# Optimization experiments

Measured on AMD Instinct MI355X. Metric: run time of the kernel, lower is better.

## Reference

```python
import jax, jax.numpy as jnp
import numpy as np

IN, HID, BATCH = 1024, 1024, 4096


def _linear_params(key, out_dim, in_dim):
    # torch.nn.Linear default init: U(-1/sqrt(in), 1/sqrt(in))
    k1, k2 = jax.random.split(key)
    bound = 1.0 / np.sqrt(in_dim)
    w = jax.random.uniform(k1, (out_dim, in_dim), jnp.float32, -bound, bound)
    b = jax.random.uniform(k2, (out_dim,), jnp.float32, -bound, bound)
    return w, b


def setup_inputs() -> dict:
    key = jax.random.key(0)
    keys = jax.random.split(key, 11)
    inp = {
        'input': jax.random.normal(keys[0], (BATCH, IN), jnp.float32),
        'h': jax.random.normal(keys[1], (BATCH, HID), jnp.float32),
        'c': jax.random.normal(keys[2], (BATCH, HID), jnp.float32),
    }
    names = ['i_i', 'i_h', 'f_i', 'f_h', 'g_i', 'g_h', 'o_i', 'o_h']
    for n, k in zip(names, keys[3:]):
        in_dim = IN if n.endswith('_i') else HID
        w, b = _linear_params(k, HID, in_dim)
        inp['w_' + n] = w
        inp['b_' + n] = b
    return inp


def reference(input, h, c,
              w_i_i, b_i_i, w_i_h, b_i_h,
              w_f_i, b_f_i, w_f_h, b_f_h,
              w_g_i, b_g_i, w_g_h, b_g_h,
              w_o_i, b_o_i, w_o_h, b_o_h):
    def lin(x, w, b):
        return x @ w.T + b

    i = jax.nn.sigmoid(lin(input, w_i_i, b_i_i) + lin(h, w_i_h, b_i_h))
    f = jax.nn.sigmoid(lin(input, w_f_i, b_f_i) + lin(h, w_f_h, b_f_h))
    g = jnp.tanh(lin(input, w_g_i, b_g_i) + lin(h, w_g_h, b_g_h))
    o = jax.nn.sigmoid(lin(input, w_o_i, b_o_i) + lin(h, w_o_h, b_o_h))
    c_prime = f * c + i * g
    h_prime = o * jnp.tanh(c_prime)
    return (h_prime, c_prime)
```

## Files before the change

### kernel.cpp

```cpp
#include <hip/hip_runtime.h>
#include <stdint.h>

#define BATCH 4096
#define IN_DIM 1024
#define HID 1024
#define KDIM 2048
#define NGATE 4096

typedef __attribute__((ext_vector_type(4))) float floatx4;
typedef __attribute__((ext_vector_type(8))) __bf16 bf16x8;

__device__ __forceinline__ unsigned short f2bf(float f) {
    union { float f; unsigned int u; } v; v.f = f;
    unsigned int u = v.u;
    u += 0x7fffu + ((u >> 16) & 1u);
    return (unsigned short)(u >> 16);
}
__device__ __forceinline__ float bf2f(unsigned short s) {
    union { unsigned int u; float f; } v; v.u = ((unsigned int)s) << 16;
    return v.f;
}

__global__ void prep_kernel(
    const float* __restrict__ x,  const float* __restrict__ h,
    const float* __restrict__ wii, const float* __restrict__ wih,
    const float* __restrict__ wfi, const float* __restrict__ wfh,
    const float* __restrict__ wgi, const float* __restrict__ wgh,
    const float* __restrict__ woi, const float* __restrict__ woh,
    const float* __restrict__ bii, const float* __restrict__ bih,
    const float* __restrict__ bfi, const float* __restrict__ bfh,
    const float* __restrict__ bgi, const float* __restrict__ bgh,
    const float* __restrict__ boi, const float* __restrict__ boh,
    unsigned short* __restrict__ Xb,
    unsigned short* __restrict__ Wb,
    float* __restrict__ bias)
{
    const int t = blockIdx.x * blockDim.x + threadIdx.x;
    const int XV = BATCH * KDIM / 4;
    if (t < XV) {
        const int e = t * 4;
        const int b = e >> 11, k = e & 2047;
        const float* src = (k < IN_DIM) ? (x + (size_t)b * IN_DIM + k)
                                        : (h + (size_t)b * HID + (k - IN_DIM));
        float4 v = *(const float4*)src;
        ushort4 o = { f2bf(v.x), f2bf(v.y), f2bf(v.z), f2bf(v.w) };
        *(ushort4*)(Xb + e) = o;
    } else if (t < 2 * XV) {
        const int e = (t - XV) * 4;
        const int r = e >> 11, k = e & 2047;
        const int gate = r >> 10, n = r & 1023;
        const float* wi_[4] = { wii, wfi, wgi, woi };
        const float* wh_[4] = { wih, wfh, wgh, woh };
        const float* src = (k < IN_DIM) ? (wi_[gate] + (size_t)n * IN_DIM + k)
                                        : (wh_[gate] + (size_t)n * HID + (k - IN_DIM));
        float4 v = *(const float4*)src;
        ushort4 o = { f2bf(v.x), f2bf(v.y), f2bf(v.z), f2bf(v.w) };
        *(ushort4*)(Wb + e) = o;
    }
    if (t < NGATE) {
        const int gate = t >> 10, n = t & 1023;
        const float* bi_[4] = { bii, bfi, bgi, boi };
        const float* bh_[4] = { bih, bfh, bgh, boh };
        bias[t] = bi_[gate][n] + bh_[gate][n];
    }
}

#define GLD16(g, l)                                                          \
    __builtin_amdgcn_global_load_lds(                                        \
        (__attribute__((address_space(1))) void*)(g),                        \
        (__attribute__((address_space(3))) void*)(l), 16, 0, 0)

__global__ __launch_bounds__(256) void gemm_gates(
    const unsigned short* __restrict__ X,
    const unsigned short* __restrict__ W,
    const float* __restrict__ bias,
    unsigned short* __restrict__ G)
{
    __shared__ __align__(16) unsigned short As[128 * 32];
    __shared__ __align__(16) unsigned short Bs[128 * 32];

    const int tid  = threadIdx.x;
    const int wave = tid >> 6;
    const int lane = tid & 63;
    const int quad = lane >> 4, idx = lane & 15;
    const int wm = (wave >> 1) * 64, wn = (wave & 1) * 64;

    const int rowA0 = blockIdx.x * 128;
    const int rowB0 = blockIdx.y * 128;

    const int srow = tid >> 2, skk = (tid & 3) * 8;
    const unsigned short* gA0 = X + (size_t)(rowA0 + srow) * KDIM + skk;
    const unsigned short* gA1 = X + (size_t)(rowA0 + 64 + srow) * KDIM + skk;
    const unsigned short* gB0 = W + (size_t)(rowB0 + srow) * KDIM + skk;
    const unsigned short* gB1 = W + (size_t)(rowB0 + 64 + srow) * KDIM + skk;

    floatx4 acc[4][4] = {};

    for (int k0 = 0; k0 < KDIM; k0 += 32) {
        GLD16(gA0 + k0, As + tid * 8);
        GLD16(gA1 + k0, As + 2048 + tid * 8);
        GLD16(gB0 + k0, Bs + tid * 8);
        GLD16(gB1 + k0, Bs + 2048 + tid * 8);
        __syncthreads();

        bf16x8 af[4], bfr[4];
#pragma unroll
        for (int i = 0; i < 4; ++i)
            af[i] = *(const bf16x8*)(As + (wm + i * 16 + idx) * 32 + quad * 8);
#pragma unroll
        for (int j = 0; j < 4; ++j)
            bfr[j] = *(const bf16x8*)(Bs + (wn + j * 16 + idx) * 32 + quad * 8);
#pragma unroll
        for (int i = 0; i < 4; ++i)
#pragma unroll
            for (int j = 0; j < 4; ++j)
                acc[i][j] = __builtin_amdgcn_mfma_f32_16x16x32_bf16(
                    af[i], bfr[j], acc[i][j], 0, 0, 0);
        __syncthreads();
    }

#pragma unroll
    for (int j = 0; j < 4; ++j) {
        const int col = rowB0 + wn + j * 16 + idx;
        const float bv = bias[col];
        const int gate = col >> 10;
#pragma unroll
        for (int i = 0; i < 4; ++i) {
#pragma unroll
            for (int r = 0; r < 4; ++r) {
                const int row = rowA0 + wm + i * 16 + quad * 4 + r;
                const float v = acc[i][j][r] + bv;
                float a;
                if (gate == 2) {
                    const float e = __expf(2.f * v);
                    a = (e - 1.f) / (e + 1.f);
                } else {
                    a = 1.f / (1.f + __expf(-v));
                }
                G[(size_t)row * NGATE + col] = f2bf(a);
            }
        }
    }
}

__global__ void ew_kernel(const unsigned short* __restrict__ G,
                          const float* __restrict__ c,
                          float* __restrict__ out)
{
    const int t = blockIdx.x * blockDim.x + threadIdx.x;
    const int b = t >> 10, n = t & 1023;
    const unsigned short* g = G + (size_t)b * NGATE;
    const float iv = bf2f(g[n]);
    const float fv = bf2f(g[HID + n]);
    const float gv = bf2f(g[2 * HID + n]);
    const float ov = bf2f(g[3 * HID + n]);
    const float cv = c[t];
    const float cp = fv * cv + iv * gv;
    const float e  = __expf(2.f * cp);
    const float th = (e - 1.f) / (e + 1.f);
    out[t] = ov * th;
    out[(size_t)BATCH * HID + t] = cp;
}

extern "C" void kernel_launch(void* const* d_in, const int* in_sizes, int n_in,
                              void* d_out, int out_size, void* d_ws, size_t ws_size,
                              hipStream_t stream) {
    const float* x   = (const float*)d_in[0];
    const float* h   = (const float*)d_in[1];
    const float* c   = (const float*)d_in[2];
    const float* wii = (const float*)d_in[3];
    const float* bii = (const float*)d_in[4];
    const float* wih = (const float*)d_in[5];
    const float* bih = (const float*)d_in[6];
    const float* wfi = (const float*)d_in[7];
    const float* bfi = (const float*)d_in[8];
    const float* wfh = (const float*)d_in[9];
    const float* bfh = (const float*)d_in[10];
    const float* wgi = (const float*)d_in[11];
    const float* bgi = (const float*)d_in[12];
    const float* wgh = (const float*)d_in[13];
    const float* bgh = (const float*)d_in[14];
    const float* woi = (const float*)d_in[15];
    const float* boi = (const float*)d_in[16];
    const float* woh = (const float*)d_in[17];
    const float* boh = (const float*)d_in[18];

    char* ws = (char*)d_ws;
    unsigned short* Xb  = (unsigned short*)ws;
    unsigned short* Wb  = (unsigned short*)(ws + ((size_t)16 << 20));
    float*          bsv = (float*)(ws + ((size_t)32 << 20));
    unsigned short* G   = (unsigned short*)(ws + ((size_t)32 << 20) + 65536);

    const int prep_threads = 2 * BATCH * KDIM / 4;
    prep_kernel<<<(prep_threads + 255) / 256, 256, 0, stream>>>(
        x, h, wii, wih, wfi, wfh, wgi, wgh, woi, woh,
        bii, bih, bfi, bfh, bgi, bgh, boi, boh, Xb, Wb, bsv);

    dim3 g2(BATCH / 128, NGATE / 128);
    gemm_gates<<<g2, 256, 0, stream>>>(Xb, Wb, bsv, G);

    ew_kernel<<<(BATCH * HID + 255) / 256, 256, 0, stream>>>(G, c, (float*)d_out);
}
```

Baseline: 261.7 us.

## Interleave gate weight rows and fuse LSTM cell update into GEMM epilogue

Reorders the packed weight and bias rows so the four gates of each hidden unit sit in adjacent columns. The GEMM epilogue can then gather i/f/g/o with lane shuffles and compute c' and h' directly, which removes the bf16 gate buffer and the separate elementwise kernel. The prep kernel also converts 8 elements per thread instead of 4. In exchange, only one lane in four stores to each output, writes are strided by the unit index, and every lane computes a redundant tanh.

```diff
diff --git a/kernel.cpp b/kernel.cpp
--- a/kernel.cpp
+++ b/kernel.cpp
@@ -9,16 +9,13 @@
 
 typedef __attribute__((ext_vector_type(4))) float floatx4;
 typedef __attribute__((ext_vector_type(8))) __bf16 bf16x8;
+typedef __attribute__((ext_vector_type(8))) unsigned short ushort8;
 
 __device__ __forceinline__ unsigned short f2bf(float f) {
     union { float f; unsigned int u; } v; v.f = f;
     unsigned int u = v.u;
     u += 0x7fffu + ((u >> 16) & 1u);
     return (unsigned short)(u >> 16);
-}
-__device__ __forceinline__ float bf2f(unsigned short s) {
-    union { unsigned int u; float f; } v; v.u = ((unsigned int)s) << 16;
-    return v.f;
 }
 
 __global__ void prep_kernel(
@@ -36,32 +33,36 @@
     float* __restrict__ bias)
 {
     const int t = blockIdx.x * blockDim.x + threadIdx.x;
-    const int XV = BATCH * KDIM / 4;
-    if (t < XV) {
-        const int e = t * 4;
+    const int XV8 = BATCH * KDIM / 8;
+    if (t < XV8) {
+        const int e = t * 8;
         const int b = e >> 11, k = e & 2047;
         const float* src = (k < IN_DIM) ? (x + (size_t)b * IN_DIM + k)
                                         : (h + (size_t)b * HID + (k - IN_DIM));
-        float4 v = *(const float4*)src;
-        ushort4 o = { f2bf(v.x), f2bf(v.y), f2bf(v.z), f2bf(v.w) };
-        *(ushort4*)(Xb + e) = o;
-    } else if (t < 2 * XV) {
-        const int e = (t - XV) * 4;
+        float4 v0 = ((const float4*)src)[0];
+        float4 v1 = ((const float4*)src)[1];
+        ushort8 o = { f2bf(v0.x), f2bf(v0.y), f2bf(v0.z), f2bf(v0.w),
+                      f2bf(v1.x), f2bf(v1.y), f2bf(v1.z), f2bf(v1.w) };
+        *(ushort8*)(Xb + e) = o;
+    } else if (t < 2 * XV8) {
+        const int e = (t - XV8) * 8;
         const int r = e >> 11, k = e & 2047;
-        const int gate = r >> 10, n = r & 1023;
+        const int u = r >> 2, gate = r & 3;
         const float* wi_[4] = { wii, wfi, wgi, woi };
         const float* wh_[4] = { wih, wfh, wgh, woh };
-        const float* src = (k < IN_DIM) ? (wi_[gate] + (size_t)n * IN_DIM + k)
-                                        : (wh_[gate] + (size_t)n * HID + (k - IN_DIM));
-        float4 v = *(const float4*)src;
-        ushort4 o = { f2bf(v.x), f2bf(v.y), f2bf(v.z), f2bf(v.w) };
-        *(ushort4*)(Wb + e) = o;
+        const float* src = (k < IN_DIM) ? (wi_[gate] + (size_t)u * IN_DIM + k)
+                                        : (wh_[gate] + (size_t)u * HID + (k - IN_DIM));
+        float4 v0 = ((const float4*)src)[0];
+        float4 v1 = ((const float4*)src)[1];
+        ushort8 o = { f2bf(v0.x), f2bf(v0.y), f2bf(v0.z), f2bf(v0.w),
+                      f2bf(v1.x), f2bf(v1.y), f2bf(v1.z), f2bf(v1.w) };
+        *(ushort8*)(Wb + e) = o;
     }
     if (t < NGATE) {
-        const int gate = t >> 10, n = t & 1023;
+        const int u = t >> 2, g = t & 3;
         const float* bi_[4] = { bii, bfi, bgi, boi };
         const float* bh_[4] = { bih, bfh, bgh, boh };
-        bias[t] = bi_[gate][n] + bh_[gate][n];
+        bias[t] = bi_[g][u] + bh_[g][u];
     }
 }
 
@@ -70,11 +71,12 @@
         (__attribute__((address_space(1))) void*)(g),                        \
         (__attribute__((address_space(3))) void*)(l), 16, 0, 0)
 
-__global__ __launch_bounds__(256) void gemm_gates(
+__global__ __launch_bounds__(256) void gemm_lstm(
     const unsigned short* __restrict__ X,
     const unsigned short* __restrict__ W,
     const float* __restrict__ bias,
-    unsigned short* __restrict__ G)
+    const float* __restrict__ c_in,
+    float* __restrict__ out)
 {
     __shared__ __align__(16) unsigned short As[128 * 32];
     __shared__ __align__(16) unsigned short Bs[128 * 32];
@@ -119,47 +121,39 @@
         __syncthreads();
     }
 
+    const int g = idx & 3;
+    const int lbase = lane & ~3;
+    float* __restrict__ out_h = out;
+    float* __restrict__ out_c = out + (size_t)BATCH * HID;
+
 #pragma unroll
     for (int j = 0; j < 4; ++j) {
         const int col = rowB0 + wn + j * 16 + idx;
+        const int u = col >> 2;
         const float bv = bias[col];
-        const int gate = col >> 10;
 #pragma unroll
         for (int i = 0; i < 4; ++i) {
 #pragma unroll
             for (int r = 0; r < 4; ++r) {
                 const int row = rowA0 + wm + i * 16 + quad * 4 + r;
                 const float v = acc[i][j][r] + bv;
-                float a;
-                if (gate == 2) {
-                    const float e = __expf(2.f * v);
-                    a = (e - 1.f) / (e + 1.f);
-                } else {
-                    a = 1.f / (1.f + __expf(-v));
-                }
-                G[(size_t)row * NGATE + col] = f2bf(a);
+                const float vv = (g == 2) ? 2.f * v : v;
+                const float s  = 1.f / (1.f + __expf(-vv));
+                const float a  = (g == 2) ? 2.f * s - 1.f : s;
+                const float iv = __shfl(a, lbase + 0, 64);
+                const float fv = __shfl(a, lbase + 1, 64);
+                const float gv = __shfl(a, lbase + 2, 64);
+                const float ov = __shfl(a, lbase + 3, 64);
+                const float cv = c_in[(size_t)row * HID + u];
+                const float cp = fv * cv + iv * gv;
+                const float e2 = __expf(2.f * cp);
+                const float th = (e2 - 1.f) / (e2 + 1.f);
+                const float hp = ov * th;
+                if (g == 0)      out_h[(size_t)row * HID + u] = hp;
+                else if (g == 1) out_c[(size_t)row * HID + u] = cp;
             }
         }
     }
-}
-
-__global__ void ew_kernel(const unsigned short* __restrict__ G,
-                          const float* __restrict__ c,
-                          float* __restrict__ out)
-{
-    const int t = blockIdx.x * blockDim.x + threadIdx.x;
-    const int b = t >> 10, n = t & 1023;
-    const unsigned short* g = G + (size_t)b * NGATE;
-    const float iv = bf2f(g[n]);
-    const float fv = bf2f(g[HID + n]);
-    const float gv = bf2f(g[2 * HID + n]);
-    const float ov = bf2f(g[3 * HID + n]);
-    const float cv = c[t];
-    const float cp = fv * cv + iv * gv;
-    const float e  = __expf(2.f * cp);
-    const float th = (e - 1.f) / (e + 1.f);
-    out[t] = ov * th;
-    out[(size_t)BATCH * HID + t] = cp;
 }
 
 extern "C" void kernel_launch(void* const* d_in, const int* in_sizes, int n_in,
@@ -189,15 +183,12 @@
     unsigned short* Xb  = (unsigned short*)ws;
     unsigned short* Wb  = (unsigned short*)(ws + ((size_t)16 << 20));
     float*          bsv = (float*)(ws + ((size_t)32 << 20));
-    unsigned short* G   = (unsigned short*)(ws + ((size_t)32 << 20) + 65536);
 
-    const int prep_threads = 2 * BATCH * KDIM / 4;
+    const int prep_threads = 2 * BATCH * KDIM / 8;
     prep_kernel<<<(prep_threads + 255) / 256, 256, 0, stream>>>(
         x, h, wii, wih, wfi, wfh, wgi, wgh, woi, woh,
         bii, bih, bfi, bfh, bgi, bgh, boi, boh, Xb, Wb, bsv);
 
     dim3 g2(BATCH / 128, NGATE / 128);
-    gemm_gates<<<g2, 256, 0, stream>>>(Xb, Wb, bsv, G);
-
-    ew_kernel<<<(BATCH * HID + 255) / 256, 256, 0, stream>>>(G, c, (float*)d_out);
+    gemm_lstm<<<g2, 256, 0, stream>>>(Xb, Wb, bsv, c, (float*)d_out);
 }
```

New measurement: 293.7 us. 12.2% more time.
